# Performance work log

Measured on AMD Instinct MI355X. Metric: run time of the kernel, lower is better.

## Reference

```python
import jax, jax.numpy as jnp
import numpy as np

L = 50            # self.length
ARG = 5           # argument_limit
OUT = 3 * L + 5   # output_size = 155
VOC = 100         # max_embeddings
B = 4096          # batch of formulas
LEAVES = 64       # predicate leaves per tree (depth-6 binary tree)
LEVEL_OFFSETS = [0, 32, 48, 56, 60, 62]  # op_ids offsets, bottom-up levels


def setup_inputs() -> dict:
    key = jax.random.key(0)
    ks = jax.random.split(key, 12)
    s = 0.05
    return {
        "pred_ids": jax.random.randint(ks[0], (B, LEAVES), 0, VOC),
        "arg_ids": jax.random.randint(ks[1], (B, LEAVES, ARG), 0, VOC),
        "op_ids": jax.random.randint(ks[2], (B, LEAVES - 1), 0, VOC),
        "emb_pred": jax.random.normal(ks[3], (VOC, L), jnp.float32),
        "emb_var": jax.random.normal(ks[4], (VOC, L), jnp.float32),
        "emb_op": jax.random.normal(ks[5], (VOC, L), jnp.float32),
        "W_pred": jax.random.normal(ks[6], (L, (1 + ARG) * L), jnp.float32) * s,
        "b_pred": jnp.zeros((L,), jnp.float32),
        "W_bin": jax.random.normal(ks[7], (L, 3 * L), jnp.float32) * s,
        "b_bin": jnp.zeros((L,), jnp.float32),
        "W_final": jax.random.normal(ks[8], (OUT, L), jnp.float32) * s,
        "b_final": jnp.zeros((OUT,), jnp.float32),
    }


def reference(pred_ids, arg_ids, op_ids, emb_pred, emb_var, emb_op,
              W_pred, b_pred, W_bin, b_bin, W_final, b_final):
    # Leaf terms: plain embedding lookup (visit_encoded_element)
    args = emb_var[arg_ids]                         # [B, LEAVES, ARG, L]
    pred = emb_pred[pred_ids]                       # [B, LEAVES, L]
    cat = jnp.concatenate([pred, args.reshape(B, LEAVES, ARG * L)], axis=-1)
    # visit_predicate_expression: relu(Linear(concat))
    x = jax.nn.relu(cat @ W_pred.T + b_pred)        # [B, LEAVES, L]
    # Bottom-up binary-formula levels: relu(Linear(concat(left, op, right)))
    for off in LEVEL_OFFSETS:
        n = x.shape[1] // 2
        left, right = x[:, 0::2], x[:, 1::2]        # [B, n, L]
        op = emb_op[op_ids[:, off:off + n]]         # [B, n, L]
        x = jax.nn.relu(
            jnp.concatenate([left, op, right], axis=-1) @ W_bin.T + b_bin)
    # forward: self.final(self.visit(input)) at tree root
    return x[:, 0] @ W_final.T + b_final            # [B, OUT]
```

## Files before the change

### kernel.cpp

```cpp
#include <hip/hip_runtime.h>

using short8 = __attribute__((ext_vector_type(8))) short;
using h8     = __attribute__((ext_vector_type(8))) _Float16;
using h2     = __attribute__((ext_vector_type(2))) _Float16;
using f32x4  = __attribute__((ext_vector_type(4))) float;

#define NB  16
#define NTH 512
#define WBIN_OFF 0
#define WFIN_OFF 12288
#define EMBO_OFF 22528
#define LTAB_OFF 28928
#define WS_USHORTS 67328

__device__ __forceinline__ unsigned short f2h_bits(float v) {
    _Float16 h = (_Float16)v;
    return *reinterpret_cast<unsigned short*>(&h);
}
__device__ __forceinline__ h8 ld8h(const unsigned short* p) {
    return *reinterpret_cast<const h8*>(p);
}
__device__ __forceinline__ short8 ld8s(const unsigned short* p) {
    return *reinterpret_cast<const short8*>(p);
}
__device__ __forceinline__ f32x4 mf(h8 a, h8 b, f32x4 c) {
    return __builtin_amdgcn_mfma_f32_16x16x32_f16(a, b, c, 0, 0, 0);
}

__global__ void prep_kernel(const float* __restrict__ emb_pred,
                            const float* __restrict__ emb_var,
                            const float* __restrict__ emb_op,
                            const float* __restrict__ W_pred,
                            const float* __restrict__ W_bin,
                            const float* __restrict__ W_final,
                            unsigned short* __restrict__ ws) {
    for (int i = blockIdx.x * blockDim.x + threadIdx.x; i < WS_USHORTS;
         i += gridDim.x * blockDim.x) {
        float v = 0.f;
        if (i < WFIN_OFF) {
            int n = i / 192, k = i - n * 192, p = k >> 6, j = k & 63;
            if (n < 50 && j < 50) v = W_bin[n * 150 + p * 50 + j];
        } else if (i < EMBO_OFF) {
            int t = i - WFIN_OFF, o = t >> 6, k = t & 63;
            if (o < 155 && k < 50) v = W_final[o * 50 + k];
        } else if (i < LTAB_OFF) {
            int t = i - EMBO_OFF, r = t >> 6, j = t & 63;
            if (j < 50) v = emb_op[r * 50 + j];
        } else {
            int t = i - LTAB_OFF;
            int p = t / 6400, rest = t - p * 6400, vv = rest >> 6, n = rest & 63;
            if (n < 50) {
                const float* e = (p == 0) ? (emb_pred + vv * 50) : (emb_var + vv * 50);
                const float* wr = W_pred + n * 300 + p * 50;
                float acc = 0.f;
                for (int k = 0; k < 50; ++k) acc += e[k] * wr[k];
                v = acc;
            }
        }
        ws[i] = f2h_bits(v);
    }
}

#define TNODE(NT0, NTN, CL, CR, GN, DST) do {                                   \
    const unsigned short* rl_ = s_x[CL];                                        \
    const unsigned short* rr_ = s_x[CR];                                        \
    int r_ = s_op[(GN) * 16 + l15];                                             \
    h8 aL0 = ld8h(rl_ + l15 * 64 + ((quad ^ (l15 & 7)) << 3));                  \
    h8 aL1 = ld8h(rl_ + l15 * 64 + (((quad + 4) ^ (l15 & 7)) << 3));            \
    h8 aO0 = ld8h(s_embop + r_ * 64 + ((quad ^ (r_ & 7)) << 3));                \
    h8 aO1 = ld8h(s_embop + r_ * 64 + (((quad + 4) ^ (r_ & 7)) << 3));          \
    h8 aR0 = ld8h(rr_ + l15 * 64 + ((quad ^ (l15 & 7)) << 3));                  \
    h8 aR1 = ld8h(rr_ + l15 * 64 + (((quad + 4) ^ (l15 & 7)) << 3));            \
    f32x4 acc_[NTN];                                                            \
    _Pragma("unroll") for (int i_ = 0; i_ < (NTN); ++i_) {                      \
        acc_[i_] = (f32x4){0.f, 0.f, 0.f, 0.f};                                 \
        acc_[i_] = mf(aL0, wb[0][0][(NT0) + i_], acc_[i_]);                     \
        acc_[i_] = mf(aL1, wb[0][1][(NT0) + i_], acc_[i_]);                     \
        acc_[i_] = mf(aO0, wb[1][0][(NT0) + i_], acc_[i_]);                     \
        acc_[i_] = mf(aO1, wb[1][1][(NT0) + i_], acc_[i_]);                     \
        acc_[i_] = mf(aR0, wb[2][0][(NT0) + i_], acc_[i_]);                     \
        acc_[i_] = mf(aR1, wb[2][1][(NT0) + i_], acc_[i_]);                     \
    }                                                                           \
    unsigned short* drow_ = s_x[DST];                                           \
    _Pragma("unroll") for (int i_ = 0; i_ < (NTN); ++i_) {                      \
        int n_ = ((NT0) + i_) * 16 + l15;                                       \
        _Pragma("unroll") for (int q_ = 0; q_ < 4; ++q_) {                      \
            int m_ = quad * 4 + q_;                                             \
            float v_ = fmaxf(acc_[i_][q_] + biasb[(NT0) + i_], 0.f);            \
            drow_[m_ * 64 + (((n_ >> 3) ^ (m_ & 7)) << 3) + (n_ & 7)] = f2h_bits(v_); \
        }                                                                       \
    }                                                                           \
} while (0)

__global__ __launch_bounds__(NTH, 2) void formula_kernel(
    const int* __restrict__ pred_ids, const int* __restrict__ arg_ids,
    const int* __restrict__ op_ids,
    const float* __restrict__ b_pred, const float* __restrict__ b_bin,
    const float* __restrict__ b_final,
    const unsigned short* __restrict__ ws,
    float* __restrict__ out)
{
    __shared__ __align__(16) unsigned short s_x[64][1024];
    __shared__ __align__(16) unsigned short s_embop[100 * 64];
    __shared__ __align__(8)  unsigned char  s_ids[64][16][8];
    __shared__ unsigned char s_op[63 * 16 + 16];

    const int tid  = threadIdx.x;
    const int b0   = blockIdx.x * NB;
    const int lane = tid & 63;
    const int w    = tid >> 6;
    const int l15  = lane & 15;
    const int quad = lane >> 4;
    const int cg   = tid & 7;

    for (int i = tid; i < 800; i += NTH) {
        int r = i >> 3, s = i & 7;
        *reinterpret_cast<short8*>(&s_embop[r * 64 + ((s ^ (r & 7)) << 3)]) =
            ld8s(ws + EMBO_OFF + r * 64 + s * 8);
    }
    for (int e = tid; e < 64 * 16; e += NTH) {
        int m = e >> 6, lf = e & 63;
        unsigned char* rec = &s_ids[lf][m][0];
        rec[0] = (unsigned char)pred_ids[(b0 + m) * 64 + lf];
        #pragma unroll
        for (int a = 0; a < 5; ++a)
            rec[1 + a] = (unsigned char)arg_ids[(b0 + m) * 320 + lf * 5 + a];
        rec[6] = 0; rec[7] = 0;
    }
    for (int e = tid; e < 63 * 16; e += NTH) {
        int r = e >> 4, m = e & 15;
        s_op[r * 16 + m] = (unsigned char)op_ids[(b0 + m) * 63 + r];
    }

    short8 wb_raw[3][2][4];
    #pragma unroll
    for (int p = 0; p < 3; ++p)
        #pragma unroll
        for (int h = 0; h < 2; ++h)
            #pragma unroll
            for (int nt = 0; nt < 4; ++nt)
                wb_raw[p][h][nt] = ld8s(ws + WBIN_OFF + (nt * 16 + l15) * 192
                                        + p * 64 + (quad + 4 * h) * 8);
    h8 (&wb)[3][2][4] = reinterpret_cast<h8(&)[3][2][4]>(wb_raw);

    float biasb[4];
    #pragma unroll
    for (int nt = 0; nt < 4; ++nt) {
        int n = nt * 16 + l15;
        biasb[nt] = (n < 50) ? b_bin[n] : 0.f;
    }
    h2 bias2[4];
    #pragma unroll
    for (int k = 0; k < 4; ++k) {
        int n0 = cg * 8 + 2 * k, n1 = n0 + 1;
        bias2[k] = (h2){(_Float16)((n0 < 50) ? b_pred[n0] : 0.f),
                        (_Float16)((n1 < 50) ? b_pred[n1] : 0.f)};
    }
    const h2 z2 = (h2){(_Float16)0.f, (_Float16)0.f};

    __syncthreads();

    #pragma unroll 4
    for (int p4 = 0; p4 < 16; ++p4) {
        int jj  = p4 * NTH + tid;
        int lf  = jj >> 7;
        int m   = (jj >> 3) & 15;
        const unsigned int* ivp =
            reinterpret_cast<const unsigned int*>(&s_ids[lf][m][0]);
        unsigned int ix = ivp[0], iy = ivp[1];
        int r0 = ix & 255, r1 = (ix >> 8) & 255, r2 = (ix >> 16) & 255;
        int r3 = ix >> 24, r4 = iy & 255, r5 = (iy >> 8) & 255;
        h2 a0 = bias2[0], a1 = bias2[1], a2 = bias2[2], a3 = bias2[3];
        #define ACCT(ROW, P) {                                                  \
            h8 t_ = ld8h(ws + LTAB_OFF + (P) * 6400 + (ROW) * 64 + cg * 8);     \
            const h2* tp_ = reinterpret_cast<const h2*>(&t_);                   \
            a0 += tp_[0]; a1 += tp_[1]; a2 += tp_[2]; a3 += tp_[3]; }
        ACCT(r0, 0); ACCT(r1, 1); ACCT(r2, 2);
        ACCT(r3, 3); ACCT(r4, 4); ACCT(r5, 5);
        #undef ACCT
        a0 = __builtin_elementwise_max(a0, z2);
        a1 = __builtin_elementwise_max(a1, z2);
        a2 = __builtin_elementwise_max(a2, z2);
        a3 = __builtin_elementwise_max(a3, z2);
        union { h2 h[4]; short8 s; } u;
        u.h[0] = a0; u.h[1] = a1; u.h[2] = a2; u.h[3] = a3;
        *reinterpret_cast<short8*>(
            &s_x[lf][m * 64 + ((cg ^ (m & 7)) << 3)]) = u.s;
    }
    __syncthreads();

    #pragma unroll
    for (int i = 0; i < 4; ++i) {
        int j = w + 8 * i;
        TNODE(0, 4, 2 * j, 2 * j + 1, j, 2 * j);
    }
    __syncthreads();
    #pragma unroll
    for (int i = 0; i < 2; ++i) {
        int j = w + 8 * i;
        TNODE(0, 4, 4 * j, 4 * j + 2, 32 + j, 4 * j);
    }
    __syncthreads();
    { int j = w; TNODE(0, 4, 8 * j, 8 * j + 4, 48 + j, 8 * j); }
    __syncthreads();
    {
        int j = w >> 1;
        if ((w & 1) == 0) TNODE(0, 2, 16 * j, 16 * j + 8, 56 + j, 16 * j + 1);
        else              TNODE(2, 2, 16 * j, 16 * j + 8, 56 + j, 16 * j + 1);
    }
    __syncthreads();
    {
        int j = w >> 2;
        switch (w & 3) {
            case 0: TNODE(0, 1, 32 * j + 1, 32 * j + 17, 60 + j, 32 * j + 2); break;
            case 1: TNODE(1, 1, 32 * j + 1, 32 * j + 17, 60 + j, 32 * j + 2); break;
            case 2: TNODE(2, 1, 32 * j + 1, 32 * j + 17, 60 + j, 32 * j + 2); break;
            default: TNODE(3, 1, 32 * j + 1, 32 * j + 17, 60 + j, 32 * j + 2); break;
        }
    }
    __syncthreads();
    if (w < 4) {
        switch (w) {
            case 0: TNODE(0, 1, 2, 34, 62, 1); break;
            case 1: TNODE(1, 1, 2, 34, 62, 1); break;
            case 2: TNODE(2, 1, 2, 34, 62, 1); break;
            default: TNODE(3, 1, 2, 34, 62, 1); break;
        }
    }
    __syncthreads();

    auto headtile = [&](int t) {
        f32x4 acc = {0.f, 0.f, 0.f, 0.f};
        int n2 = t * 16 + l15;
        const unsigned short* rroot = s_x[1];
        h8 x0 = ld8h(rroot + l15 * 64 + ((quad ^ (l15 & 7)) << 3));
        h8 x1 = ld8h(rroot + l15 * 64 + (((quad + 4) ^ (l15 & 7)) << 3));
        acc = mf(x0, ld8h(ws + WFIN_OFF + n2 * 64 + quad * 8), acc);
        acc = mf(x1, ld8h(ws + WFIN_OFF + n2 * 64 + (quad + 4) * 8), acc);
        if (n2 < 155) {
            float bias = b_final[n2];
            #pragma unroll
            for (int q = 0; q < 4; ++q) {
                int m = quad * 4 + q;
                out[(b0 + m) * 155 + n2] = acc[q] + bias;
            }
        }
    };
    headtile(w);
    if (w < 2) headtile(8 + w);
}

extern "C" void kernel_launch(void* const* d_in, const int* in_sizes, int n_in,
                              void* d_out, int out_size, void* d_ws, size_t ws_size,
                              hipStream_t stream) {
    const int*   pred_ids = (const int*)  d_in[0];
    const int*   arg_ids  = (const int*)  d_in[1];
    const int*   op_ids   = (const int*)  d_in[2];
    const float* emb_pred = (const float*)d_in[3];
    const float* emb_var  = (const float*)d_in[4];
    const float* emb_op   = (const float*)d_in[5];
    const float* W_pred   = (const float*)d_in[6];
    const float* b_pred   = (const float*)d_in[7];
    const float* W_bin    = (const float*)d_in[8];
    const float* b_bin    = (const float*)d_in[9];
    const float* W_final  = (const float*)d_in[10];
    const float* b_final  = (const float*)d_in[11];
    unsigned short* ws = (unsigned short*)d_ws;
    float* out = (float*)d_out;

    hipLaunchKernelGGL(prep_kernel, dim3(256), dim3(256), 0, stream,
                       emb_pred, emb_var, emb_op, W_pred, W_bin, W_final, ws);
    hipLaunchKernelGGL(formula_kernel, dim3(4096 / NB), dim3(NTH), 0, stream,
                       pred_ids, arg_ids, op_ids, b_pred, b_bin, b_final,
                       (const unsigned short*)ws, out);
}
```

Measured before the change: 31.83 us.

## Precombine leaf projection tables into pairwise sum tables to halve gathers

Adds a prep kernel that builds three 100x100 pair tables, each holding the fp16 sum of two adjacent per-slot leaf projection rows. The leaf stage then does three gathers per leaf instead of six. This trades leaf-stage gather loads and adds for an extra launch that writes about 3.8 MB of tables. Leaf gathers then hit a table too large to stay in cache, and rounding the pair sums to fp16 changes numerics slightly.

```diff
diff --git a/kernel.cpp b/kernel.cpp
--- a/kernel.cpp
+++ b/kernel.cpp
@@ -12,6 +12,8 @@
 #define EMBO_OFF 22528
 #define LTAB_OFF 28928
 #define WS_USHORTS 67328
+#define PAIR_OFF 67328
+#define PAIR_STRIDE 640000
 
 __device__ __forceinline__ unsigned short f2h_bits(float v) {
     _Float16 h = (_Float16)v;
@@ -61,6 +63,27 @@
     }
 }
 
+__global__ void prep2_kernel(unsigned short* __restrict__ ws) {
+    const unsigned short* base = ws + LTAB_OFF;
+    unsigned short* pt = ws + PAIR_OFF;
+    const int total = 3 * 10000 * 8;
+    for (int t = blockIdx.x * blockDim.x + threadIdx.x; t < total;
+         t += gridDim.x * blockDim.x) {
+        int p   = t / 80000;
+        int rem = t - p * 80000;
+        int row = rem >> 3;
+        int s   = rem & 7;
+        int i   = row / 100, j = row - i * 100;
+        h8 a = ld8h(base + (2 * p) * 6400 + i * 64 + s * 8);
+        h8 b = ld8h(base + (2 * p + 1) * 6400 + j * 64 + s * 8);
+        h8 r;
+        #pragma unroll
+        for (int e = 0; e < 8; ++e)
+            r[e] = (_Float16)((float)a[e] + (float)b[e]);
+        *reinterpret_cast<h8*>(pt + p * PAIR_STRIDE + row * 64 + s * 8) = r;
+    }
+}
+
 #define TNODE(NT0, NTN, CL, CR, GN, DST) do {                                   \
     const unsigned short* rl_ = s_x[CL];                                        \
     const unsigned short* rr_ = s_x[CR];                                        \
@@ -170,14 +193,14 @@
         unsigned int ix = ivp[0], iy = ivp[1];
         int r0 = ix & 255, r1 = (ix >> 8) & 255, r2 = (ix >> 16) & 255;
         int r3 = ix >> 24, r4 = iy & 255, r5 = (iy >> 8) & 255;
+        int q0 = r0 * 100 + r1, q1 = r2 * 100 + r3, q2 = r4 * 100 + r5;
         h2 a0 = bias2[0], a1 = bias2[1], a2 = bias2[2], a3 = bias2[3];
-        #define ACCT(ROW, P) {                                                  \
-            h8 t_ = ld8h(ws + LTAB_OFF + (P) * 6400 + (ROW) * 64 + cg * 8);     \
+        #define PACCT(Q, P) {                                                   \
+            h8 t_ = ld8h(ws + PAIR_OFF + (P) * PAIR_STRIDE + (Q) * 64 + cg * 8);\
             const h2* tp_ = reinterpret_cast<const h2*>(&t_);                   \
             a0 += tp_[0]; a1 += tp_[1]; a2 += tp_[2]; a3 += tp_[3]; }
-        ACCT(r0, 0); ACCT(r1, 1); ACCT(r2, 2);
-        ACCT(r3, 3); ACCT(r4, 4); ACCT(r5, 5);
-        #undef ACCT
+        PACCT(q0, 0); PACCT(q1, 1); PACCT(q2, 2);
+        #undef PACCT
         a0 = __builtin_elementwise_max(a0, z2);
         a1 = __builtin_elementwise_max(a1, z2);
         a2 = __builtin_elementwise_max(a2, z2);
@@ -270,6 +293,7 @@
 
     hipLaunchKernelGGL(prep_kernel, dim3(256), dim3(256), 0, stream,
                        emb_pred, emb_var, emb_op, W_pred, W_bin, W_final, ws);
+    hipLaunchKernelGGL(prep2_kernel, dim3(512), dim3(256), 0, stream, ws);
     hipLaunchKernelGGL(formula_kernel, dim3(4096 / NB), dim3(NTH), 0, stream,
                        pred_ids, arg_ids, op_ids, b_pred, b_bin, b_final,
                        (const unsigned short*)ws, out);
```

Result: slower. 37.86 us (+18.9%).

## Stage leaf lookup tables in LDS and process tree in two half-subtrees

Applied to the files above, without the earlier changes.

Copies the six fused leaf lookup tables (about 77KB) into shared memory so the leaf stage gathers from LDS rather than global/L2. To free space, the per-leaf activation buffer is cut from 64 to 35 rows by running the tree in two 32-leaf halves, with the two half roots stored in spare rows and combined at the end. The op-embedding table is now read straight from global memory inside each node. This adds a large LDS preload per block, which likely drops occupancy to one block per CU, and it adds more barriers.

```diff
diff --git a/kernel.cpp b/kernel.cpp
--- a/kernel.cpp
+++ b/kernel.cpp
@@ -67,8 +67,8 @@
     int r_ = s_op[(GN) * 16 + l15];                                             \
     h8 aL0 = ld8h(rl_ + l15 * 64 + ((quad ^ (l15 & 7)) << 3));                  \
     h8 aL1 = ld8h(rl_ + l15 * 64 + (((quad + 4) ^ (l15 & 7)) << 3));            \
-    h8 aO0 = ld8h(s_embop + r_ * 64 + ((quad ^ (r_ & 7)) << 3));                \
-    h8 aO1 = ld8h(s_embop + r_ * 64 + (((quad + 4) ^ (r_ & 7)) << 3));          \
+    h8 aO0 = ld8h(ws + EMBO_OFF + r_ * 64 + quad * 8);                          \
+    h8 aO1 = ld8h(ws + EMBO_OFF + r_ * 64 + (quad + 4) * 8);                    \
     h8 aR0 = ld8h(rr_ + l15 * 64 + ((quad ^ (l15 & 7)) << 3));                  \
     h8 aR1 = ld8h(rr_ + l15 * 64 + (((quad + 4) ^ (l15 & 7)) << 3));            \
     f32x4 acc_[NTN];                                                            \
@@ -100,8 +100,8 @@
     const unsigned short* __restrict__ ws,
     float* __restrict__ out)
 {
-    __shared__ __align__(16) unsigned short s_x[64][1024];
-    __shared__ __align__(16) unsigned short s_embop[100 * 64];
+    __shared__ __align__(16) unsigned short s_ltab[6 * 100 * 64];
+    __shared__ __align__(16) unsigned short s_x[35][1024];
     __shared__ __align__(8)  unsigned char  s_ids[64][16][8];
     __shared__ unsigned char s_op[63 * 16 + 16];
 
@@ -113,11 +113,8 @@
     const int quad = lane >> 4;
     const int cg   = tid & 7;
 
-    for (int i = tid; i < 800; i += NTH) {
-        int r = i >> 3, s = i & 7;
-        *reinterpret_cast<short8*>(&s_embop[r * 64 + ((s ^ (r & 7)) << 3)]) =
-            ld8s(ws + EMBO_OFF + r * 64 + s * 8);
-    }
+    for (int i = tid; i < 4800; i += NTH)
+        *reinterpret_cast<short8*>(&s_ltab[i * 8]) = ld8s(ws + LTAB_OFF + i * 8);
     for (int e = tid; e < 64 * 16; e += NTH) {
         int m = e >> 6, lf = e & 63;
         unsigned char* rec = &s_ids[lf][m][0];
@@ -160,71 +157,76 @@
 
     __syncthreads();
 
-    #pragma unroll 4
-    for (int p4 = 0; p4 < 16; ++p4) {
-        int jj  = p4 * NTH + tid;
-        int lf  = jj >> 7;
-        int m   = (jj >> 3) & 15;
-        const unsigned int* ivp =
-            reinterpret_cast<const unsigned int*>(&s_ids[lf][m][0]);
-        unsigned int ix = ivp[0], iy = ivp[1];
-        int r0 = ix & 255, r1 = (ix >> 8) & 255, r2 = (ix >> 16) & 255;
-        int r3 = ix >> 24, r4 = iy & 255, r5 = (iy >> 8) & 255;
-        h2 a0 = bias2[0], a1 = bias2[1], a2 = bias2[2], a3 = bias2[3];
-        #define ACCT(ROW, P) {                                                  \
-            h8 t_ = ld8h(ws + LTAB_OFF + (P) * 6400 + (ROW) * 64 + cg * 8);     \
-            const h2* tp_ = reinterpret_cast<const h2*>(&t_);                   \
-            a0 += tp_[0]; a1 += tp_[1]; a2 += tp_[2]; a3 += tp_[3]; }
-        ACCT(r0, 0); ACCT(r1, 1); ACCT(r2, 2);
-        ACCT(r3, 3); ACCT(r4, 4); ACCT(r5, 5);
-        #undef ACCT
-        a0 = __builtin_elementwise_max(a0, z2);
-        a1 = __builtin_elementwise_max(a1, z2);
-        a2 = __builtin_elementwise_max(a2, z2);
-        a3 = __builtin_elementwise_max(a3, z2);
-        union { h2 h[4]; short8 s; } u;
-        u.h[0] = a0; u.h[1] = a1; u.h[2] = a2; u.h[3] = a3;
-        *reinterpret_cast<short8*>(
-            &s_x[lf][m * 64 + ((cg ^ (m & 7)) << 3)]) = u.s;
-    }
-    __syncthreads();
-
-    #pragma unroll
-    for (int i = 0; i < 4; ++i) {
-        int j = w + 8 * i;
-        TNODE(0, 4, 2 * j, 2 * j + 1, j, 2 * j);
-    }
-    __syncthreads();
-    #pragma unroll
-    for (int i = 0; i < 2; ++i) {
-        int j = w + 8 * i;
-        TNODE(0, 4, 4 * j, 4 * j + 2, 32 + j, 4 * j);
-    }
-    __syncthreads();
-    { int j = w; TNODE(0, 4, 8 * j, 8 * j + 4, 48 + j, 8 * j); }
-    __syncthreads();
-    {
-        int j = w >> 1;
-        if ((w & 1) == 0) TNODE(0, 2, 16 * j, 16 * j + 8, 56 + j, 16 * j + 1);
-        else              TNODE(2, 2, 16 * j, 16 * j + 8, 56 + j, 16 * j + 1);
-    }
-    __syncthreads();
-    {
-        int j = w >> 2;
-        switch (w & 3) {
-            case 0: TNODE(0, 1, 32 * j + 1, 32 * j + 17, 60 + j, 32 * j + 2); break;
-            case 1: TNODE(1, 1, 32 * j + 1, 32 * j + 17, 60 + j, 32 * j + 2); break;
-            case 2: TNODE(2, 1, 32 * j + 1, 32 * j + 17, 60 + j, 32 * j + 2); break;
-            default: TNODE(3, 1, 32 * j + 1, 32 * j + 17, 60 + j, 32 * j + 2); break;
-        }
-    }
-    __syncthreads();
+    for (int c = 0; c < 2; ++c) {
+        #pragma unroll 4
+        for (int p4 = 0; p4 < 8; ++p4) {
+            int jj  = p4 * NTH + tid;
+            int lfl = jj >> 7;
+            int m   = (jj >> 3) & 15;
+            const unsigned int* ivp =
+                reinterpret_cast<const unsigned int*>(&s_ids[c * 32 + lfl][m][0]);
+            unsigned int ix = ivp[0], iy = ivp[1];
+            int r0 = ix & 255, r1 = (ix >> 8) & 255, r2 = (ix >> 16) & 255;
+            int r3 = ix >> 24, r4 = iy & 255, r5 = (iy >> 8) & 255;
+            h2 a0 = bias2[0], a1 = bias2[1], a2 = bias2[2], a3 = bias2[3];
+            #define ACCT(ROW, P) {                                              \
+                h8 t_ = ld8h(s_ltab + (P) * 6400 + (ROW) * 64 + cg * 8);        \
+                const h2* tp_ = reinterpret_cast<const h2*>(&t_);               \
+                a0 += tp_[0]; a1 += tp_[1]; a2 += tp_[2]; a3 += tp_[3]; }
+            ACCT(r0, 0); ACCT(r1, 1); ACCT(r2, 2);
+            ACCT(r3, 3); ACCT(r4, 4); ACCT(r5, 5);
+            #undef ACCT
+            a0 = __builtin_elementwise_max(a0, z2);
+            a1 = __builtin_elementwise_max(a1, z2);
+            a2 = __builtin_elementwise_max(a2, z2);
+            a3 = __builtin_elementwise_max(a3, z2);
+            union { h2 h[4]; short8 s; } u;
+            u.h[0] = a0; u.h[1] = a1; u.h[2] = a2; u.h[3] = a3;
+            *reinterpret_cast<short8*>(
+                &s_x[lfl][m * 64 + ((cg ^ (m & 7)) << 3)]) = u.s;
+        }
+        __syncthreads();
+
+        #pragma unroll
+        for (int i = 0; i < 2; ++i) {
+            int j = w + 8 * i;
+            TNODE(0, 4, 2 * j, 2 * j + 1, c * 16 + j, 2 * j);
+        }
+        __syncthreads();
+        { int j = w; TNODE(0, 4, 4 * j, 4 * j + 2, 32 + c * 8 + j, 4 * j); }
+        __syncthreads();
+        {
+            int j = w >> 1;
+            if ((w & 1) == 0) TNODE(0, 2, 8 * j, 8 * j + 4, 48 + c * 4 + j, 8 * j + 1);
+            else              TNODE(2, 2, 8 * j, 8 * j + 4, 48 + c * 4 + j, 8 * j + 1);
+        }
+        __syncthreads();
+        {
+            int j = w >> 2;
+            switch (w & 3) {
+                case 0: TNODE(0, 1, 16 * j + 1, 16 * j + 9, 56 + c * 2 + j, 16 * j + 2); break;
+                case 1: TNODE(1, 1, 16 * j + 1, 16 * j + 9, 56 + c * 2 + j, 16 * j + 2); break;
+                case 2: TNODE(2, 1, 16 * j + 1, 16 * j + 9, 56 + c * 2 + j, 16 * j + 2); break;
+                default: TNODE(3, 1, 16 * j + 1, 16 * j + 9, 56 + c * 2 + j, 16 * j + 2); break;
+            }
+        }
+        __syncthreads();
+        if (w < 4) {
+            switch (w) {
+                case 0: TNODE(0, 1, 2, 18, 60 + c, 32 + c); break;
+                case 1: TNODE(1, 1, 2, 18, 60 + c, 32 + c); break;
+                case 2: TNODE(2, 1, 2, 18, 60 + c, 32 + c); break;
+                default: TNODE(3, 1, 2, 18, 60 + c, 32 + c); break;
+            }
+        }
+        __syncthreads();
+    }
     if (w < 4) {
         switch (w) {
-            case 0: TNODE(0, 1, 2, 34, 62, 1); break;
-            case 1: TNODE(1, 1, 2, 34, 62, 1); break;
-            case 2: TNODE(2, 1, 2, 34, 62, 1); break;
-            default: TNODE(3, 1, 2, 34, 62, 1); break;
+            case 0: TNODE(0, 1, 32, 33, 62, 34); break;
+            case 1: TNODE(1, 1, 32, 33, 62, 34); break;
+            case 2: TNODE(2, 1, 32, 33, 62, 34); break;
+            default: TNODE(3, 1, 32, 33, 62, 34); break;
         }
     }
     __syncthreads();
@@ -232,7 +234,7 @@
     auto headtile = [&](int t) {
         f32x4 acc = {0.f, 0.f, 0.f, 0.f};
         int n2 = t * 16 + l15;
-        const unsigned short* rroot = s_x[1];
+        const unsigned short* rroot = s_x[34];
         h8 x0 = ld8h(rroot + l15 * 64 + ((quad ^ (l15 & 7)) << 3));
         h8 x1 = ld8h(rroot + l15 * 64 + (((quad + 4) ^ (l15 & 7)) << 3));
         acc = mf(x0, ld8h(ws + WFIN_OFF + n2 * 64 + quad * 8), acc);
```

Result: slower. 39.81 us (+25.1%).
